# Kernel optimization log

Hardware: AMD Instinct MI355X
Metric: run time of the kernel (lower is better)

The kernel has to match this reference:

```python
import jax, jax.numpy as jnp
import numpy as np

B, T, D, H = 64, 2048, 256, 5


def setup_inputs() -> dict:
    key = jax.random.key(0)
    ks = jax.random.split(key, 4)
    return {
        "x_temp": jax.random.normal(ks[0], (B, T, D), dtype=jnp.float32),
        "x_fea": jax.random.normal(ks[1], (B, T), dtype=jnp.float32),
        "mask": jnp.ones((B, T), dtype=bool),
        "W_temp": jax.random.normal(ks[2], (D, H), dtype=jnp.float32) * 0.05,
        "b_temp": jnp.zeros((H,), dtype=jnp.float32),
        "W_fea": jax.random.normal(ks[3], (1, H), dtype=jnp.float32) * 0.05,
        "b_fea": jnp.zeros((H,), dtype=jnp.float32),
        "b": jnp.zeros((H,), dtype=jnp.float32),
        "uw": jax.random.normal(jax.random.fold_in(key, 7), (H, H), dtype=jnp.float32) * 0.05,
    }


def reference(x_temp, x_fea, mask, W_temp, b_temp, W_fea, b_fea, b, uw):
    # temp: (B,T,H) projection of features
    temp = jnp.einsum("btd,dh->bth", x_temp, W_temp) + b_temp
    # fea: (B,T,H) projection of the scalar per-timestep feature
    fea = x_fea[..., None] * W_fea[0] + b_fea
    hadamard = jnp.tanh(temp) * jnp.tanh(fea)            # (B,T,H)
    intermed = jnp.sum(hadamard @ uw + b, axis=-1)       # (B,T)
    weights = jax.nn.softmax(intermed, axis=-1)          # (B,T)
    m = mask.astype(jnp.float32)
    weights = weights * m
    weights = weights / jnp.sum(weights, axis=-1, keepdims=True)
    return jnp.sum(x_temp * weights[..., None], axis=1)  # (B,D)
```

## Files before the change

kernel.cpp:

```cpp
#include <hip/hip_runtime.h>
#include <hip/hip_bf16.h>
#include <math.h>

constexpr int BB   = 64;
constexpr int TT   = 2048;
constexpr int DD   = 256;
constexpr int HH   = 5;
constexpr int SEG  = 64;
constexpr int TSEG = TT / SEG;
constexpr int PSTR = 260;

__device__ __forceinline__ float ftanh(float x) {
    float e = __expf(2.0f * x);
    return 1.0f - 2.0f * __builtin_amdgcn_rcpf(e + 1.0f);
}

template <int CTRL>
__device__ __forceinline__ float dpp_add(float x) {
    int s = __builtin_amdgcn_update_dpp(0, __float_as_int(x), CTRL, 0xf, 0xf, true);
    return x + __int_as_float(s);
}
__device__ __forceinline__ float half_sum_dpp(float v) {
    v = dpp_add<0x111>(v);
    v = dpp_add<0x112>(v);
    v = dpp_add<0x114>(v);
    v = dpp_add<0x118>(v);
    v = dpp_add<0x142>(v);
    return v;
}

__global__ __launch_bounds__(256, 4)
void seg_kernel(const float* __restrict__ x_temp,
                const float* __restrict__ x_fea,
                const int* __restrict__ mask,
                const float* __restrict__ W_temp,
                const float* __restrict__ b_temp,
                const float* __restrict__ W_fea,
                const float* __restrict__ b_fea,
                const float* __restrict__ uw,
                float* __restrict__ part)
{
    __shared__ alignas(16) float im[2 * TSEG];
    __shared__ alignas(16) float ldsw[8 * 264];

    const int tid  = threadIdx.x;
    const int l    = tid & 63;
    const int wave = tid >> 6;
    const int half = l >> 5;
    const int l32  = l & 31;
    const int blk  = blockIdx.x;
    const int b    = blk >> 6;
    const int seg  = blk & (SEG - 1);
    const int t0   = seg * TSEG;
    const size_t rowbase = (size_t)b * TT;
    const float* xbase = x_temp + (rowbase + t0) * (size_t)DD;

    if (tid < TSEG) im[2 * tid + 1] = mask[rowbase + t0 + tid] ? 1.0f : 0.0f;

    const int dbase = l32 * 8;
    float4 xq[4][2];
#pragma unroll
    for (int it = 0; it < 4; ++it) {
        const float* p = xbase + it * (8 * DD) + wave * (2 * DD) + half * DD + dbase;
        xq[it][0] = *(const float4*)(p);
        xq[it][1] = *(const float4*)(p + 4);
    }

    float wv[8][HH];
#pragma unroll
    for (int e = 0; e < 8; ++e)
#pragma unroll
        for (int h = 0; h < HH; ++h)
            wv[e][h] = W_temp[(dbase + e) * HH + h];

    float wfea[HH], bfea[HH], btmp[HH], uwr[HH];
#pragma unroll
    for (int h = 0; h < HH; ++h) {
        wfea[h] = W_fea[h]; bfea[h] = b_fea[h]; btmp[h] = b_temp[h];
        float s = 0.f;
#pragma unroll
        for (int h2 = 0; h2 < HH; ++h2) s += uw[h * HH + h2];
        uwr[h] = s;
    }

#pragma unroll
    for (int it = 0; it < 4; ++it) {
        const int r = it * 8 + wave * 2 + half;
        const float4 a0 = xq[it][0], a1 = xq[it][1];
        float ph[HH];
#pragma unroll
        for (int h = 0; h < HH; ++h)
            ph[h] = a0.x * wv[0][h] + a0.y * wv[1][h] + a0.z * wv[2][h] + a0.w * wv[3][h]
                  + a1.x * wv[4][h] + a1.y * wv[5][h] + a1.z * wv[6][h] + a1.w * wv[7][h];
#pragma unroll
        for (int h = 0; h < HH; ++h)
            ph[h] = half_sum_dpp(ph[h]);

        if (l32 == 31) {
            const float xf = x_fea[rowbase + t0 + r];
            float inter = 0.f;
#pragma unroll
            for (int h = 0; h < HH; ++h)
                inter += ftanh(ph[h] + btmp[h]) * ftanh(xf * wfea[h] + bfea[h]) * uwr[h];
            im[2 * r] = inter;
        }
    }
    __syncthreads();

    float lsum = 0.f;
#pragma unroll
    for (int k = 0; k < 16; ++k) {
        float4 v = *(const float4*)(&im[4 * k]);
        lsum += v.y * __expf(v.x) + v.w * __expf(v.z);
    }

    float acc8[8] = {0.f, 0.f, 0.f, 0.f, 0.f, 0.f, 0.f, 0.f};
#pragma unroll
    for (int it = 0; it < 4; ++it) {
        const int r = it * 8 + wave * 2 + half;
        const float w = im[2 * r + 1] * __expf(im[2 * r]);
        const float4 a0 = xq[it][0], a1 = xq[it][1];
        acc8[0] = fmaf(w, a0.x, acc8[0]); acc8[1] = fmaf(w, a0.y, acc8[1]);
        acc8[2] = fmaf(w, a0.z, acc8[2]); acc8[3] = fmaf(w, a0.w, acc8[3]);
        acc8[4] = fmaf(w, a1.x, acc8[4]); acc8[5] = fmaf(w, a1.y, acc8[5]);
        acc8[6] = fmaf(w, a1.z, acc8[6]); acc8[7] = fmaf(w, a1.w, acc8[7]);
    }

    const int slot = wave * 2 + half;
    float* wp = &ldsw[slot * 264 + dbase];
    *(float4*)(wp)     = make_float4(acc8[0], acc8[1], acc8[2], acc8[3]);
    *(float4*)(wp + 4) = make_float4(acc8[4], acc8[5], acc8[6], acc8[7]);
    __syncthreads();

    float accd = 0.f;
#pragma unroll
    for (int s = 0; s < 8; ++s) accd += ldsw[s * 264 + tid];

    float* pb = part + (size_t)blk * PSTR;
    if (tid == 0) pb[0] = lsum;
    pb[1 + tid] = accd;
}

__global__ __launch_bounds__(256)
void combine_kernel(const float* __restrict__ part, float* __restrict__ out)
{
    const int b = blockIdx.x;
    const int d = threadIdx.x;
    const float* base = part + (size_t)b * SEG * PSTR;
    float den = 0.f, num = 0.f;
#pragma unroll 8
    for (int s = 0; s < SEG; ++s) {
        const float* p = base + (size_t)s * PSTR;
        den += p[0];
        num += p[1 + d];
    }
    out[(size_t)b * DD + d] = num / den;
}

extern "C" void kernel_launch(void* const* d_in, const int* in_sizes, int n_in,
                              void* d_out, int out_size, void* d_ws, size_t ws_size,
                              hipStream_t stream) {
    const float* x_temp = (const float*)d_in[0];
    const float* x_fea  = (const float*)d_in[1];
    const int*   mask   = (const int*)d_in[2];
    const float* W_temp = (const float*)d_in[3];
    const float* b_temp = (const float*)d_in[4];
    const float* W_fea  = (const float*)d_in[5];
    const float* b_fea  = (const float*)d_in[6];
    const float* uw     = (const float*)d_in[8];

    float* part = (float*)d_ws;
    float* out  = (float*)d_out;

    seg_kernel<<<BB * SEG, 256, 0, stream>>>(x_temp, x_fea, mask, W_temp,
                                             b_temp, W_fea, b_fea, uw, part);
    combine_kernel<<<BB, DD, 0, stream>>>(part, out);
}
```

Baseline: 208.8 us.

## Spread tanh/exp scoring across threads and parallelize combine over segments

Each segment now writes the per-row projection sums to shared memory, and 32 threads compute the tanh scoring, exp weight and segment denominator in parallel. Previously one lane per row did this serially and every thread recomputed the denominator from 32 exponentials. W_temp is loaded with float4 vector loads. The combine kernel uses 1024 threads, split into four groups that each reduce 16 segments, and finishes with a shared-memory reduction. The cost is an extra barrier and a small shared buffer.

Result: no change. 205.7 us (-1.5%).

```diff
diff --git a/kernel.cpp b/kernel.cpp
--- a/kernel.cpp
+++ b/kernel.cpp
@@ -41,6 +41,8 @@
                 float* __restrict__ part)
 {
     __shared__ alignas(16) float im[2 * TSEG];
+    __shared__ alignas(16) float phl[TSEG][6];
+    __shared__ float lsh;
     __shared__ alignas(16) float ldsw[8 * 264];
 
     const int tid  = threadIdx.x;
@@ -66,59 +68,57 @@
         xq[it][1] = *(const float4*)(p + 4);
     }
 
-    float wv[8][HH];
+    float wvf[40];
+    {
+        const float4* wp = (const float4*)(W_temp + dbase * HH);
 #pragma unroll
-    for (int e = 0; e < 8; ++e)
-#pragma unroll
-        for (int h = 0; h < HH; ++h)
-            wv[e][h] = W_temp[(dbase + e) * HH + h];
-
-    float wfea[HH], bfea[HH], btmp[HH], uwr[HH];
-#pragma unroll
-    for (int h = 0; h < HH; ++h) {
-        wfea[h] = W_fea[h]; bfea[h] = b_fea[h]; btmp[h] = b_temp[h];
-        float s = 0.f;
-#pragma unroll
-        for (int h2 = 0; h2 < HH; ++h2) s += uw[h * HH + h2];
-        uwr[h] = s;
+        for (int q = 0; q < 10; ++q) ((float4*)wvf)[q] = wp[q];
     }
 
 #pragma unroll
     for (int it = 0; it < 4; ++it) {
         const int r = it * 8 + wave * 2 + half;
         const float4 a0 = xq[it][0], a1 = xq[it][1];
-        float ph[HH];
 #pragma unroll
-        for (int h = 0; h < HH; ++h)
-            ph[h] = a0.x * wv[0][h] + a0.y * wv[1][h] + a0.z * wv[2][h] + a0.w * wv[3][h]
-                  + a1.x * wv[4][h] + a1.y * wv[5][h] + a1.z * wv[6][h] + a1.w * wv[7][h];
-#pragma unroll
-        for (int h = 0; h < HH; ++h)
-            ph[h] = half_sum_dpp(ph[h]);
-
-        if (l32 == 31) {
-            const float xf = x_fea[rowbase + t0 + r];
-            float inter = 0.f;
-#pragma unroll
-            for (int h = 0; h < HH; ++h)
-                inter += ftanh(ph[h] + btmp[h]) * ftanh(xf * wfea[h] + bfea[h]) * uwr[h];
-            im[2 * r] = inter;
+        for (int h = 0; h < HH; ++h) {
+            float ph = a0.x * wvf[0 * HH + h] + a0.y * wvf[1 * HH + h]
+                     + a0.z * wvf[2 * HH + h] + a0.w * wvf[3 * HH + h]
+                     + a1.x * wvf[4 * HH + h] + a1.y * wvf[5 * HH + h]
+                     + a1.z * wvf[6 * HH + h] + a1.w * wvf[7 * HH + h];
+            ph = half_sum_dpp(ph);
+            if (l32 == 31) phl[r][h] = ph;
         }
     }
     __syncthreads();
 
-    float lsum = 0.f;
+    if (tid < TSEG) {
+        const int r = tid;
+        float wfea[HH], bfea[HH], btmp[HH], uwr[HH];
 #pragma unroll
-    for (int k = 0; k < 16; ++k) {
-        float4 v = *(const float4*)(&im[4 * k]);
-        lsum += v.y * __expf(v.x) + v.w * __expf(v.z);
+        for (int h = 0; h < HH; ++h) {
+            wfea[h] = W_fea[h]; bfea[h] = b_fea[h]; btmp[h] = b_temp[h];
+            float s = 0.f;
+#pragma unroll
+            for (int h2 = 0; h2 < HH; ++h2) s += uw[h * HH + h2];
+            uwr[h] = s;
+        }
+        const float xf = x_fea[rowbase + t0 + r];
+        float inter = 0.f;
+#pragma unroll
+        for (int h = 0; h < HH; ++h)
+            inter += ftanh(phl[r][h] + btmp[h]) * ftanh(xf * wfea[h] + bfea[h]) * uwr[h];
+        const float e = im[2 * r + 1] * __expf(inter);
+        im[2 * r] = e;
+        const float ls = half_sum_dpp(e);
+        if (r == 31) lsh = ls;
     }
+    __syncthreads();
 
     float acc8[8] = {0.f, 0.f, 0.f, 0.f, 0.f, 0.f, 0.f, 0.f};
 #pragma unroll
     for (int it = 0; it < 4; ++it) {
         const int r = it * 8 + wave * 2 + half;
-        const float w = im[2 * r + 1] * __expf(im[2 * r]);
+        const float w = im[2 * r];
         const float4 a0 = xq[it][0], a1 = xq[it][1];
         acc8[0] = fmaf(w, a0.x, acc8[0]); acc8[1] = fmaf(w, a0.y, acc8[1]);
         acc8[2] = fmaf(w, a0.z, acc8[2]); acc8[3] = fmaf(w, a0.w, acc8[3]);
@@ -137,24 +137,34 @@
     for (int s = 0; s < 8; ++s) accd += ldsw[s * 264 + tid];
 
     float* pb = part + (size_t)blk * PSTR;
-    if (tid == 0) pb[0] = lsum;
+    if (tid == 0) pb[0] = lsh;
     pb[1 + tid] = accd;
 }
 
-__global__ __launch_bounds__(256)
+__global__ __launch_bounds__(1024)
 void combine_kernel(const float* __restrict__ part, float* __restrict__ out)
 {
+    __shared__ float red[4 * DD];
+    __shared__ float dred[4];
     const int b = blockIdx.x;
-    const int d = threadIdx.x;
+    const int d = threadIdx.x & (DD - 1);
+    const int g = threadIdx.x >> 8;
     const float* base = part + (size_t)b * SEG * PSTR;
     float den = 0.f, num = 0.f;
-#pragma unroll 8
-    for (int s = 0; s < SEG; ++s) {
-        const float* p = base + (size_t)s * PSTR;
+#pragma unroll
+    for (int s = 0; s < 16; ++s) {
+        const float* p = base + (size_t)(g * 16 + s) * PSTR;
         den += p[0];
         num += p[1 + d];
     }
-    out[(size_t)b * DD + d] = num / den;
+    red[g * DD + d] = num;
+    if (d == 0) dred[g] = den;
+    __syncthreads();
+    if (g == 0) {
+        const float n  = red[d] + red[DD + d] + red[2 * DD + d] + red[3 * DD + d];
+        const float dn = dred[0] + dred[1] + dred[2] + dred[3];
+        out[(size_t)b * DD + d] = n / dn;
+    }
 }
 
 extern "C" void kernel_launch(void* const* d_in, const int* in_sizes, int n_in,
@@ -174,5 +184,5 @@
 
     seg_kernel<<<BB * SEG, 256, 0, stream>>>(x_temp, x_fea, mask, W_temp,
                                              b_temp, W_fea, b_fea, uw, part);
-    combine_kernel<<<BB, DD, 0, stream>>>(part, out);
+    combine_kernel<<<BB, 1024, 0, stream>>>(part, out);
 }
```
